# Kernel tuning notes

Measured on AMD Instinct MI355X. Metric: run time of the kernel, lower is better.

## Reference

```python
import jax, jax.numpy as jnp
import numpy as np

B, T, CIN = 8, 4096, 512
GROUP, ENTRY = 2, 320
COUT = 512
D = COUT // GROUP  # per-group codebook dim = 256


def setup_inputs() -> dict:
    key = jax.random.key(0)
    k_x, k_w, k_cb, k_g = jax.random.split(key, 4)
    x = jax.random.normal(k_x, (B, T, CIN), dtype=jnp.float32)
    # weight_proj: Linear(in_channel, group*entry)
    Wp = jax.random.normal(k_w, (GROUP * ENTRY, CIN), dtype=jnp.float32) * (1.0 / np.sqrt(CIN))
    bp = jnp.zeros((GROUP * ENTRY,), dtype=jnp.float32)
    # stacked codebooks: [group, entry, out_channel//group]
    codebooks = jax.random.normal(k_cb, (GROUP, ENTRY, D), dtype=jnp.float32)
    # pre-sampled gumbel noise (torch gumbel_softmax samples this internally)
    gumbel = jax.random.gumbel(k_g, (B, T, GROUP * ENTRY), dtype=jnp.float32)
    return {"x": x, "Wp": Wp, "bp": bp, "codebooks": codebooks, "gumbel": gumbel}


def reference(x, Wp, bp, codebooks, gumbel):
    # weight_proj
    logits = jnp.einsum('btc,ec->bte', x, Wp) + bp          # [B,T,group*entry]
    # gumbel_softmax(tau=1, hard=False, dim=-1): softmax over full group*entry axis
    y = jax.nn.softmax(logits + gumbel, axis=-1)            # [B,T,group*entry]
    # chunk into groups -> contiguous reshape matches torch.chunk
    yg = y.reshape(B, T, GROUP, ENTRY)                      # [B,T,G,E]
    # per-group matmul against codebook weights, then concat over groups
    out = jnp.einsum('btge,ged->btgd', yg, codebooks)       # [B,T,G,D]
    return out.reshape(B, T, GROUP * D)                     # [B,T,out_channel]
```

## Files before the change

### kernel.cpp

```cpp
#include <hip/hip_runtime.h>
#include <hip/hip_bf16.h>
#include <stdint.h>

#define BT     32768
#define CIN    512
#define NE     640
#define ENTRY  320
#define DD     256
#define MROWS  32
#define TPB    256

using bf16x8 = __attribute__((ext_vector_type(8))) short;
using f32x4  = __attribute__((ext_vector_type(4))) float;

#define A_OFF   0
#define A_STR   80
#define B_OFF   2560
#define Y_OFF   0
#define Y_STR   648
#define S_OFF   41472
#define CB_OFF  41600
#define SMEM_BYTES 74368

__device__ __forceinline__ unsigned short f2b(float f) {
    union { float f; uint32_t u; } v; v.f = f;
    uint32_t u = v.u;
    return (unsigned short)((u + 0x7FFFu + ((u >> 16) & 1u)) >> 16);
}

__device__ __forceinline__ void gl2lds16(const void* g, void* l) {
    __builtin_amdgcn_global_load_lds((const __attribute__((address_space(1))) void*)g,
                                     (__attribute__((address_space(3))) void*)l, 16, 0, 0);
}

__global__ void prep_kernel(const float* __restrict__ Wp, const float* __restrict__ cb,
                            unsigned short* __restrict__ WpB, unsigned short* __restrict__ cbT) {
    int i = blockIdx.x * blockDim.x + threadIdx.x;
    if (i < NE * CIN) {
        WpB[i] = f2b(Wp[i]);
    } else {
        int o = i - NE * CIN;
        if (o < 2 * ENTRY * DD) {
            int g = o / (DD * ENTRY);
            int r = o - g * (DD * ENTRY);
            int d = r / ENTRY;
            int e = r - d * ENTRY;
            cbT[o] = f2b(cb[(g * ENTRY + e) * DD + d]);
        }
    }
}

__global__ __launch_bounds__(TPB, 2) void fused_kernel(
    const float* __restrict__ x, const float* __restrict__ bp,
    const float* __restrict__ gum, const unsigned short* __restrict__ WpB,
    const unsigned short* __restrict__ cbT, float* __restrict__ out) {

    extern __shared__ char smem[];
    unsigned short* yS = (unsigned short*)(smem + Y_OFF);
    float*          sS = (float*)(smem + S_OFF);
    char*           aS = smem + A_OFF;
    char*           bS = smem + B_OFF;
    char*           cS = smem + CB_OFF;

    const int tid = threadIdx.x;
    const int w  = tid >> 6;
    const int l  = tid & 63;
    const int q  = l >> 4;
    const int ln = l & 15;
    const int rowbase = blockIdx.x * MROWS;

    f32x4 acc1[2][10];
    const f32x4 fz = {0.f, 0.f, 0.f, 0.f};
#pragma unroll
    for (int rt = 0; rt < 2; ++rt)
#pragma unroll
        for (int ct = 0; ct < 10; ++ct) acc1[rt][ct] = fz;

    const int ar  = tid >> 3;
    const int akq = tid & 7;
    const float* xrow = x + (rowbase + ar) * CIN + akq * 4;

#pragma unroll 1
    for (int ks = 0; ks < 16; ++ks) {
        const int k0 = ks * 32;
        __syncthreads();
        float4 xv = *(const float4*)(xrow + k0);
        ushort4 hv;
        hv.x = f2b(xv.x); hv.y = f2b(xv.y); hv.z = f2b(xv.z); hv.w = f2b(xv.w);
        *(ushort4*)(aS + ar * A_STR + akq * 8) = hv;
#pragma unroll
        for (int i = 0; i < 10; ++i) {
            int cbase = i * 256 + (w << 6);
            int c = cbase + l;
            int e = c >> 2;
            int q2 = (c & 3) ^ ((e >> 1) & 3);
            gl2lds16(WpB + e * CIN + k0 + q2 * 8, bS + cbase * 16);
        }
        __syncthreads();
        bf16x8 af[2];
#pragma unroll
        for (int rt = 0; rt < 2; ++rt)
            af[rt] = *(const bf16x8*)(aS + (rt * 16 + ln) * A_STR + q * 16);
        bf16x8 bfr[10];
#pragma unroll
        for (int ct = 0; ct < 10; ++ct) {
            int e = w * 160 + ct * 16 + ln;
            int ch = e * 4 + (q ^ ((e >> 1) & 3));
            bfr[ct] = *(const bf16x8*)(bS + ch * 16);
        }
#pragma unroll
        for (int rt = 0; rt < 2; ++rt)
#pragma unroll
            for (int ct = 0; ct < 10; ++ct)
                acc1[rt][ct] = __builtin_amdgcn_mfma_f32_16x16x32_bf16(af[rt], bfr[ct], acc1[rt][ct], 0, 0, 0);
    }

    __syncthreads();
    if (tid < MROWS) sS[tid] = 0.0f;
    __syncthreads();

    float bpv[10];
#pragma unroll
    for (int ct = 0; ct < 10; ++ct) bpv[ct] = bp[w * 160 + ct * 16 + ln];

    const float* gbase = gum + (size_t)rowbase * NE + w * 160 + ln;
    float gv[10];
    {
        const float* p0 = gbase + (size_t)(q * 4) * NE;
#pragma unroll
        for (int ct = 0; ct < 10; ++ct) gv[ct] = p0[ct * 16];
    }
#pragma unroll
    for (int ri = 0; ri < 8; ++ri) {
        float gn[10];
        if (ri < 7) {
            int nrow = ((ri + 1) >> 2) * 16 + q * 4 + ((ri + 1) & 3);
            const float* pn = gbase + (size_t)nrow * NE;
#pragma unroll
            for (int ct = 0; ct < 10; ++ct) gn[ct] = pn[ct * 16];
        }
        int rt = ri >> 2, r = ri & 3;
        int row = rt * 16 + q * 4 + r;
        float p = 0.f;
#pragma unroll
        for (int ct = 0; ct < 10; ++ct) {
            int col = w * 160 + ct * 16 + ln;
            float v = acc1[rt][ct][r] + bpv[ct] + gv[ct];
            float e = __expf(v);
            yS[row * Y_STR + col] = f2b(e);
            p += e;
        }
        p += __shfl_xor(p, 1);
        p += __shfl_xor(p, 2);
        p += __shfl_xor(p, 4);
        p += __shfl_xor(p, 8);
        if (ln == 0) atomicAdd(&sS[row], p);
#pragma unroll
        for (int ct = 0; ct < 10; ++ct) gv[ct] = gn[ct];
    }

    f32x4 acc2[2][8];
#pragma unroll
    for (int rt = 0; rt < 2; ++rt)
#pragma unroll
        for (int ct = 0; ct < 8; ++ct) acc2[rt][ct] = fz;

    const int g  = w >> 1;
    const int nb = (w & 1) * 128;

#pragma unroll 1
    for (int ks = 0; ks < 10; ++ks) {
        const int k0 = ks * 32;
        __syncthreads();
#pragma unroll
        for (int i = 0; i < 8; ++i) {
            int cbase = i * 256 + (w << 6);
            int c = cbase + l;
            int gg = c >> 10;
            int cc = c & 1023;
            int n = cc >> 2;
            int q2 = (cc & 3) ^ ((n >> 1) & 3);
            gl2lds16(cbT + (gg * DD + n) * ENTRY + k0 + q2 * 8, cS + cbase * 16);
        }
        __syncthreads();
        bf16x8 af[2];
#pragma unroll
        for (int rt = 0; rt < 2; ++rt)
            af[rt] = *(const bf16x8*)((char*)yS + (rt * 16 + ln) * (Y_STR * 2) + (g * ENTRY + k0 + q * 8) * 2);
        bf16x8 bfr[8];
#pragma unroll
        for (int ct = 0; ct < 8; ++ct) {
            int n = nb + ct * 16 + ln;
            int ch = (g << 10) + n * 4 + (q ^ ((n >> 1) & 3));
            bfr[ct] = *(const bf16x8*)(cS + ch * 16);
        }
#pragma unroll
        for (int rt = 0; rt < 2; ++rt)
#pragma unroll
            for (int ct = 0; ct < 8; ++ct)
                acc2[rt][ct] = __builtin_amdgcn_mfma_f32_16x16x32_bf16(af[rt], bfr[ct], acc2[rt][ct], 0, 0, 0);
    }

#pragma unroll
    for (int rt = 0; rt < 2; ++rt) {
#pragma unroll
        for (int r = 0; r < 4; ++r) {
            int row = rt * 16 + q * 4 + r;
            float inv = 1.0f / sS[row];
            int orow = (rowbase + row) * 512;
#pragma unroll
            for (int ct = 0; ct < 8; ++ct) {
                int col = g * DD + nb + ct * 16 + ln;
                out[orow + col] = acc2[rt][ct][r] * inv;
            }
        }
    }
}

extern "C" void kernel_launch(void* const* d_in, const int* in_sizes, int n_in,
                              void* d_out, int out_size, void* d_ws, size_t ws_size,
                              hipStream_t stream) {
    const float* x   = (const float*)d_in[0];
    const float* Wp  = (const float*)d_in[1];
    const float* bp  = (const float*)d_in[2];
    const float* cb  = (const float*)d_in[3];
    const float* gum = (const float*)d_in[4];
    float* out = (float*)d_out;

    unsigned short* WpB = (unsigned short*)d_ws;
    unsigned short* cbT = WpB + NE * CIN;

    int prep_total = NE * CIN + 2 * ENTRY * DD;
    prep_kernel<<<(prep_total + 255) / 256, 256, 0, stream>>>(Wp, cb, WpB, cbT);

    fused_kernel<<<dim3(BT / MROWS), dim3(TPB), SMEM_BYTES, stream>>>(x, bp, gum, WpB, cbT, out);
}
```

Baseline: 251.5 us.

## Load weight B-fragments directly from global, stage full A tile once in LDS

The weight and codebook fragments are now read straight from global memory (L2-resident, since they are small and shared) into registers instead of being staged through LDS with global_load_lds. The x tile for all 512 input channels is converted to bf16 and written once into an XOR-swizzled LDS buffer before the first GEMM, and the softmax output uses a swizzled layout, so the per-k-step barriers disappear. This shrinks LDS use, which allows raising launch bounds to three blocks per CU, and the k loops are partially unrolled. The trade-off is that every wave issues redundant uncoalesced-ish global reads of the weight fragments, relying on cache bandwidth, and register pressure rises under the tighter occupancy bound.

```diff
diff --git a/kernel.cpp b/kernel.cpp
--- a/kernel.cpp
+++ b/kernel.cpp
@@ -13,24 +13,13 @@
 using bf16x8 = __attribute__((ext_vector_type(8))) short;
 using f32x4  = __attribute__((ext_vector_type(4))) float;
 
-#define A_OFF   0
-#define A_STR   80
-#define B_OFF   2560
-#define Y_OFF   0
-#define Y_STR   648
-#define S_OFF   41472
-#define CB_OFF  41600
-#define SMEM_BYTES 74368
+#define S_OFF      40960
+#define SMEM_BYTES 41088
 
 __device__ __forceinline__ unsigned short f2b(float f) {
     union { float f; uint32_t u; } v; v.f = f;
     uint32_t u = v.u;
     return (unsigned short)((u + 0x7FFFu + ((u >> 16) & 1u)) >> 16);
-}
-
-__device__ __forceinline__ void gl2lds16(const void* g, void* l) {
-    __builtin_amdgcn_global_load_lds((const __attribute__((address_space(1))) void*)g,
-                                     (__attribute__((address_space(3))) void*)l, 16, 0, 0);
 }
 
 __global__ void prep_kernel(const float* __restrict__ Wp, const float* __restrict__ cb,
@@ -50,17 +39,13 @@
     }
 }
 
-__global__ __launch_bounds__(TPB, 2) void fused_kernel(
+__global__ __launch_bounds__(TPB, 3) void fused_kernel(
     const float* __restrict__ x, const float* __restrict__ bp,
     const float* __restrict__ gum, const unsigned short* __restrict__ WpB,
     const unsigned short* __restrict__ cbT, float* __restrict__ out) {
 
     extern __shared__ char smem[];
-    unsigned short* yS = (unsigned short*)(smem + Y_OFF);
-    float*          sS = (float*)(smem + S_OFF);
-    char*           aS = smem + A_OFF;
-    char*           bS = smem + B_OFF;
-    char*           cS = smem + CB_OFF;
+    float* sS = (float*)(smem + S_OFF);
 
     const int tid = threadIdx.x;
     const int w  = tid >> 6;
@@ -68,6 +53,25 @@
     const int q  = l >> 4;
     const int ln = l & 15;
     const int rowbase = blockIdx.x * MROWS;
+    const int swz = (ln & 7) << 4;
+
+    if (tid < MROWS) sS[tid] = 0.0f;
+
+    {
+        const int ar  = tid >> 3;
+        const int akq = tid & 7;
+        const float* xrow = x + (size_t)(rowbase + ar) * CIN + akq * 4;
+        const int abase = ar * 1024;
+        const int aswz  = (ar & 7) << 4;
+#pragma unroll
+        for (int ks = 0; ks < 16; ++ks) {
+            float4 xv = *(const float4*)(xrow + ks * 32);
+            ushort4 hv;
+            hv.x = f2b(xv.x); hv.y = f2b(xv.y); hv.z = f2b(xv.z); hv.w = f2b(xv.w);
+            *(ushort4*)(smem + abase + ((ks * 64 + akq * 8) ^ aswz)) = hv;
+        }
+    }
+    __syncthreads();
 
     f32x4 acc1[2][10];
     const f32x4 fz = {0.f, 0.f, 0.f, 0.f};
@@ -76,47 +80,27 @@
 #pragma unroll
         for (int ct = 0; ct < 10; ++ct) acc1[rt][ct] = fz;
 
-    const int ar  = tid >> 3;
-    const int akq = tid & 7;
-    const float* xrow = x + (rowbase + ar) * CIN + akq * 4;
-
-#pragma unroll 1
+    int boff[10];
+#pragma unroll
+    for (int ct = 0; ct < 10; ++ct)
+        boff[ct] = (w * 160 + ct * 16 + ln) * CIN + q * 8;
+
+#pragma unroll 2
     for (int ks = 0; ks < 16; ++ks) {
-        const int k0 = ks * 32;
-        __syncthreads();
-        float4 xv = *(const float4*)(xrow + k0);
-        ushort4 hv;
-        hv.x = f2b(xv.x); hv.y = f2b(xv.y); hv.z = f2b(xv.z); hv.w = f2b(xv.w);
-        *(ushort4*)(aS + ar * A_STR + akq * 8) = hv;
-#pragma unroll
-        for (int i = 0; i < 10; ++i) {
-            int cbase = i * 256 + (w << 6);
-            int c = cbase + l;
-            int e = c >> 2;
-            int q2 = (c & 3) ^ ((e >> 1) & 3);
-            gl2lds16(WpB + e * CIN + k0 + q2 * 8, bS + cbase * 16);
-        }
-        __syncthreads();
-        bf16x8 af[2];
-#pragma unroll
-        for (int rt = 0; rt < 2; ++rt)
-            af[rt] = *(const bf16x8*)(aS + (rt * 16 + ln) * A_STR + q * 16);
+        const unsigned short* Bk = WpB + ks * 32;
         bf16x8 bfr[10];
 #pragma unroll
+        for (int ct = 0; ct < 10; ++ct)
+            bfr[ct] = *(const bf16x8*)(Bk + boff[ct]);
+        const int at = (ks * 64 + q * 16) ^ swz;
+        bf16x8 af0 = *(const bf16x8*)(smem + ln * 1024 + at);
+        bf16x8 af1 = *(const bf16x8*)(smem + ln * 1024 + 16384 + at);
+#pragma unroll
         for (int ct = 0; ct < 10; ++ct) {
-            int e = w * 160 + ct * 16 + ln;
-            int ch = e * 4 + (q ^ ((e >> 1) & 3));
-            bfr[ct] = *(const bf16x8*)(bS + ch * 16);
-        }
-#pragma unroll
-        for (int rt = 0; rt < 2; ++rt)
-#pragma unroll
-            for (int ct = 0; ct < 10; ++ct)
-                acc1[rt][ct] = __builtin_amdgcn_mfma_f32_16x16x32_bf16(af[rt], bfr[ct], acc1[rt][ct], 0, 0, 0);
-    }
-
-    __syncthreads();
-    if (tid < MROWS) sS[tid] = 0.0f;
+            acc1[0][ct] = __builtin_amdgcn_mfma_f32_16x16x32_bf16(af0, bfr[ct], acc1[0][ct], 0, 0, 0);
+            acc1[1][ct] = __builtin_amdgcn_mfma_f32_16x16x32_bf16(af1, bfr[ct], acc1[1][ct], 0, 0, 0);
+        }
+    }
     __syncthreads();
 
     float bpv[10];
@@ -141,13 +125,15 @@
         }
         int rt = ri >> 2, r = ri & 3;
         int row = rt * 16 + q * 4 + r;
+        int ybase = row * 1280;
+        int yswz  = (row & 7) << 4;
         float p = 0.f;
 #pragma unroll
         for (int ct = 0; ct < 10; ++ct) {
             int col = w * 160 + ct * 16 + ln;
             float v = acc1[rt][ct][r] + bpv[ct] + gv[ct];
             float e = __expf(v);
-            yS[row * Y_STR + col] = f2b(e);
+            *(unsigned short*)(smem + ybase + ((col * 2) ^ yswz)) = f2b(e);
             p += e;
         }
         p += __shfl_xor(p, 1);
@@ -158,6 +144,7 @@
 #pragma unroll
         for (int ct = 0; ct < 10; ++ct) gv[ct] = gn[ct];
     }
+    __syncthreads();
 
     f32x4 acc2[2][8];
 #pragma unroll
@@ -168,37 +155,26 @@
     const int g  = w >> 1;
     const int nb = (w & 1) * 128;
 
-#pragma unroll 1
+    int coff[8];
+#pragma unroll
+    for (int ct = 0; ct < 8; ++ct)
+        coff[ct] = (g * DD + nb + ct * 16 + ln) * ENTRY + q * 8;
+
+#pragma unroll 2
     for (int ks = 0; ks < 10; ++ks) {
-        const int k0 = ks * 32;
-        __syncthreads();
-#pragma unroll
-        for (int i = 0; i < 8; ++i) {
-            int cbase = i * 256 + (w << 6);
-            int c = cbase + l;
-            int gg = c >> 10;
-            int cc = c & 1023;
-            int n = cc >> 2;
-            int q2 = (cc & 3) ^ ((n >> 1) & 3);
-            gl2lds16(cbT + (gg * DD + n) * ENTRY + k0 + q2 * 8, cS + cbase * 16);
-        }
-        __syncthreads();
-        bf16x8 af[2];
-#pragma unroll
-        for (int rt = 0; rt < 2; ++rt)
-            af[rt] = *(const bf16x8*)((char*)yS + (rt * 16 + ln) * (Y_STR * 2) + (g * ENTRY + k0 + q * 8) * 2);
+        const unsigned short* Ck = cbT + ks * 32;
         bf16x8 bfr[8];
 #pragma unroll
+        for (int ct = 0; ct < 8; ++ct)
+            bfr[ct] = *(const bf16x8*)(Ck + coff[ct]);
+        const int at = (g * 640 + ks * 64 + q * 16) ^ swz;
+        bf16x8 af0 = *(const bf16x8*)(smem + ln * 1280 + at);
+        bf16x8 af1 = *(const bf16x8*)(smem + ln * 1280 + 20480 + at);
+#pragma unroll
         for (int ct = 0; ct < 8; ++ct) {
-            int n = nb + ct * 16 + ln;
-            int ch = (g << 10) + n * 4 + (q ^ ((n >> 1) & 3));
-            bfr[ct] = *(const bf16x8*)(cS + ch * 16);
-        }
-#pragma unroll
-        for (int rt = 0; rt < 2; ++rt)
-#pragma unroll
-            for (int ct = 0; ct < 8; ++ct)
-                acc2[rt][ct] = __builtin_amdgcn_mfma_f32_16x16x32_bf16(af[rt], bfr[ct], acc2[rt][ct], 0, 0, 0);
+            acc2[0][ct] = __builtin_amdgcn_mfma_f32_16x16x32_bf16(af0, bfr[ct], acc2[0][ct], 0, 0, 0);
+            acc2[1][ct] = __builtin_amdgcn_mfma_f32_16x16x32_bf16(af1, bfr[ct], acc2[1][ct], 0, 0, 0);
+        }
     }
 
 #pragma unroll
@@ -207,7 +183,7 @@
         for (int r = 0; r < 4; ++r) {
             int row = rt * 16 + q * 4 + r;
             float inv = 1.0f / sS[row];
-            int orow = (rowbase + row) * 512;
+            size_t orow = (size_t)(rowbase + row) * 512;
 #pragma unroll
             for (int ct = 0; ct < 8; ++ct) {
                 int col = g * DD + nb + ct * 16 + ln;
```

Measured after the change: 320.7 us. 1.28x slower.
